# Kernel optimization log

Hardware: AMD Instinct MI355X
Metric: run time of the kernel (lower is better)

Reference implementation:

```python
import jax, jax.numpy as jnp
import numpy as np

B, N, C, H, CLS = 16, 1024, 768, 12, 1000
M = 0.5  # amax init for alpha


def setup_inputs() -> dict:
    key = jax.random.key(0)
    k = jax.random.split(key, 7)
    x = jax.random.normal(k[0], (B, N, C), jnp.float32)
    label = jax.random.randint(k[1], (B,), 0, CLS)
    # alpha is initialized to ones*m in the module; add small noise so gating is non-trivial
    alpha = jnp.ones((CLS, 3 * C), jnp.float32) * M + 0.1 * jax.random.normal(k[2], (CLS, 3 * C), jnp.float32)
    qkv_w = jax.random.normal(k[3], (3 * C, C), jnp.float32) * 0.02
    qkv_b = jax.random.normal(k[4], (3 * C,), jnp.float32) * 0.02
    proj_w = jax.random.normal(k[5], (C, C), jnp.float32) * 0.02
    proj_b = jax.random.normal(k[6], (C,), jnp.float32) * 0.02
    return {"x": x, "label": label, "alpha": alpha, "qkv_w": qkv_w,
            "qkv_b": qkv_b, "proj_w": proj_w, "proj_b": proj_b}


def reference(x, label, alpha, qkv_w, qkv_b, proj_w, proj_b):
    b, n, c = x.shape
    h = H
    hd = c // h
    scale = hd ** -0.5
    # per-sample sigmoid gate over the 3C output rows of the qkv projection
    sig = jax.nn.sigmoid(alpha[label])  # (B, 3C)
    # F.linear(x_i, W * s_i[:,None], b * s_i) == (x_i @ W.T) * s_i + b * s_i
    qkv = jnp.einsum('bnc,dc->bnd', x, qkv_w) * sig[:, None, :] + (qkv_b * sig)[:, None, :]
    qkv = qkv.reshape(b, n, 3, h, hd).transpose(2, 0, 3, 1, 4)  # (3, B, H, N, hd)
    q, k_, v = qkv[0], qkv[1], qkv[2]
    attn = jax.nn.softmax(jnp.einsum('bhqd,bhkd->bhqk', q, k_) * scale, axis=-1)
    out = jnp.einsum('bhqk,bhkd->bhqd', attn, v)          # (B, H, N, hd)
    out = out.transpose(0, 2, 1, 3).reshape(b, n, c)       # (B, N, C)
    out = out @ proj_w.T + proj_b
    return out
```

## Files before the change

kernel.cpp:

```cpp
#include <hip/hip_runtime.h>

typedef __bf16 bf16;
typedef __attribute__((ext_vector_type(8))) __bf16 bf16x8;
typedef __attribute__((ext_vector_type(4))) float floatx4;
typedef __attribute__((ext_vector_type(8))) short short8;
typedef __attribute__((ext_vector_type(4))) short short4v;
typedef unsigned short u16;

#define B_  16
#define N_  1024
#define C_  768
#define H_  12
#define HD_ 64
#define TC_ 2304
#define QSZ (B_ * H_ * N_ * HD_)

__device__ __forceinline__ u16 f2b(float f) { bf16 h = (bf16)f; return __builtin_bit_cast(u16, h); }

typedef __attribute__((address_space(1))) const unsigned int guint;
typedef __attribute__((address_space(3))) unsigned int luint;
__device__ __forceinline__ void gl16(const u16* g, u16* l) {
    __builtin_amdgcn_global_load_lds((guint*)g, (luint*)l, 16, 0, 0);
}

__global__ __launch_bounds__(256) void cvt_swz(
    const float* __restrict__ x, const float* __restrict__ qw,
    const float* __restrict__ pw, u16* __restrict__ xb,
    u16* __restrict__ qwb, u16* __restrict__ pwb)
{
    const int gid = blockIdx.x * 256 + threadIdx.x;
    const int b   = gid & 7;
    const int rb  = gid >> 3;
    const int row = rb / 12, g = rb - row * 12;
    const float* src; u16* dst; int r;
    if (row < 16384)      { src = x;  dst = xb;  r = row; }
    else if (row < 18688) { src = qw; dst = qwb; r = row - 16384; }
    else                  { src = pw; dst = pwb; r = row - 18688; }
    const float* sp = src + (size_t)r * 768 + g * 64 + b * 8;
    floatx4 a = *(const floatx4*)sp;
    floatx4 c = *(const floatx4*)(sp + 4);
    short8 v;
    v[0] = (short)f2b(a[0]); v[1] = (short)f2b(a[1]);
    v[2] = (short)f2b(a[2]); v[3] = (short)f2b(a[3]);
    v[4] = (short)f2b(c[0]); v[5] = (short)f2b(c[1]);
    v[6] = (short)f2b(c[2]); v[7] = (short)f2b(c[3]);
    *(short8*)(dst + (size_t)r * 768 + g * 64 + (b ^ (r & 7)) * 8) = v;
}

template <int MODE>
__global__ __launch_bounds__(256, 4) void gemm_bt(
    const u16* __restrict__ A, const u16* __restrict__ W,
    const float* __restrict__ bias, const float* __restrict__ alpha,
    const int* __restrict__ label, void* __restrict__ out, u16* __restrict__ vT)
{
    __shared__ __align__(16) u16 sm[16384];
    u16* sA = sm;
    u16* sB = sm + 8192;
    const int t  = threadIdx.x;
    const int w  = t >> 6, l = t & 63;
    const int lr = l & 15, lq = l >> 4;
    const int id = blockIdx.x;
    const int xcd = id & 7, j = id >> 3;
    const int m0 = (xcd * 16 + (j & 15)) << 7;
    const int n0 = (j >> 4) << 7;
    const int wm = (w >> 1) << 6, wn = (w & 1) << 6;
    const int sw = lr & 7;

    floatx4 acc[4][4];
#pragma unroll
    for (int a = 0; a < 4; a++)
#pragma unroll
        for (int b = 0; b < 4; b++) acc[a][b] = (floatx4){0.f, 0.f, 0.f, 0.f};

    const int cx8  = (t & 7) * 8;
    const int row0 = t >> 3;

    auto a_off = [&](int r, int ks) -> int {
        const int m = m0 + r;
        if (MODE == 0) return m * 768 + ks * 64 + cx8;
        return (((m >> 10) * H_ + ks) * N_ + (m & (N_ - 1))) * HD_ + cx8;
    };

    const int nk = 12;
    for (int ks = 0; ks < nk; ++ks) {
        __syncthreads();
#pragma unroll
        for (int i = 0; i < 4; i++) {
            gl16(A + a_off(row0 + 32 * i, ks), sA + i * 2048 + t * 8);
            gl16(W + (n0 + row0 + 32 * i) * 768 + ks * 64 + cx8, sB + i * 2048 + t * 8);
        }
        __syncthreads();
#pragma unroll
        for (int kc = 0; kc < 2; kc++) {
            bf16x8 af[4], bfr[4];
#pragma unroll
            for (int mt = 0; mt < 4; mt++)
                af[mt] = *(const bf16x8*)(sA + (wm + mt * 16 + lr) * 64 + 8 * ((kc * 4 + lq) ^ sw));
#pragma unroll
            for (int nt = 0; nt < 4; nt++)
                bfr[nt] = *(const bf16x8*)(sB + (wn + nt * 16 + lr) * 64 + 8 * ((kc * 4 + lq) ^ sw));
#pragma unroll
            for (int mt = 0; mt < 4; mt++)
#pragma unroll
                for (int nt = 0; nt < 4; nt++)
                    acc[mt][nt] = __builtin_amdgcn_mfma_f32_16x16x32_bf16(af[mt], bfr[nt], acc[mt][nt], 0, 0, 0);
        }
    }

    if (MODE == 0) {
        const int b   = m0 >> 10;
        const int lab = label[b];
        const int which = (n0 >= 1536) ? 2 : (n0 >= 768 ? 1 : 0);
        if (which == 2) {
#pragma unroll
            for (int nt = 0; nt < 4; nt++) {
                const int d3   = n0 + wn + nt * 16 + lr;
                const float sg = 1.f / (1.f + __expf(-alpha[lab * TC_ + d3]));
                const float bv = bias[d3];
                const int rcol = d3 - 1536;
                const int h = rcol >> 6, dd = rcol & 63;
                u16* vp = vT + (((b * H_ + h) * HD_ + dd) << 10);
#pragma unroll
                for (int mt = 0; mt < 4; mt++) {
                    const int nb = (m0 & 1023) + wm + mt * 16 + lq * 4;
                    const int sidx = (nb & ~63) + 8 * (((nb >> 3) & 7) ^ (dd & 7)) + (nb & 7);
                    short4v pk;
#pragma unroll
                    for (int i = 0; i < 4; i++) pk[i] = (short)f2b((acc[mt][nt][i] + bv) * sg);
                    *(short4v*)(vp + sidx) = pk;
                }
            }
        } else {
            float sgv[4], bvv[4];
#pragma unroll
            for (int nt = 0; nt < 4; nt++) {
                const int d3 = n0 + wn + nt * 16 + lr;
                sgv[nt] = 1.f / (1.f + __expf(-alpha[lab * TC_ + d3]));
                bvv[nt] = bias[d3];
            }
            const int hbase = (n0 - which * 768) >> 6;
            const int nb0   = m0 & 1023;
            u16* ob = (u16*)out + which * QSZ;
#pragma unroll
            for (int p = 0; p < 2; p++) {
                __syncthreads();
                if (wm == p * 64) {
#pragma unroll
                    for (int nt = 0; nt < 4; nt++) {
                        const int c = wn + nt * 16 + lr;
#pragma unroll
                        for (int mt = 0; mt < 4; mt++)
#pragma unroll
                            for (int i = 0; i < 4; i++)
                                sm[(mt * 16 + lq * 4 + i) * 132 + c] =
                                    f2b((acc[mt][nt][i] + bvv[nt]) * sgv[nt]);
                    }
                }
                __syncthreads();
#pragma unroll
                for (int hh = 0; hh < 2; hh++) {
                    u16* dsth = ob + ((((b * H_ + hbase + hh) << 10) + nb0 + p * 64) << 6);
#pragma unroll
                    for (int mi = 0; mi < 2; mi++) {
                        const int m = (t >> 3) + 32 * mi;
                        *(short8*)(dsth + m * 64 + (t & 7) * 8) =
                            *(const short8*)(sm + m * 132 + hh * 64 + 8 * ((t & 7) ^ (m & 7)));
                    }
                }
            }
        }
    } else {
        float bvv[4];
#pragma unroll
        for (int nt = 0; nt < 4; nt++) bvv[nt] = bias[n0 + wn + nt * 16 + lr];
        __syncthreads();
        float* swf = (float*)sm + w * (16 * 68);
        const int rr = l >> 2, c0 = (l & 3) * 16;
#pragma unroll
        for (int mt = 0; mt < 4; mt++) {
#pragma unroll
            for (int nt = 0; nt < 4; nt++)
#pragma unroll
                for (int i = 0; i < 4; i++)
                    swf[(lq * 4 + i) * 68 + nt * 16 + lr] = acc[mt][nt][i] + bvv[nt];
            float* drow = (float*)out + (m0 + wm + mt * 16 + rr) * 768 + n0 + wn + c0;
#pragma unroll
            for (int jj = 0; jj < 4; jj++)
                *(floatx4*)(drow + jj * 4) = *(const floatx4*)(swf + rr * 68 + c0 + jj * 4);
        }
    }
}

__global__ __launch_bounds__(256, 4) void attn_fwd(
    u16* __restrict__ qb, const u16* __restrict__ kb, const u16* __restrict__ vtb)
{
    __shared__ __align__(16) u16 sQP[64 * 64];
    __shared__ __align__(16) u16 sK[2][64 * 64];
    __shared__ __align__(16) u16 sVt[2][64 * 64];

    const int t = threadIdx.x, w = t >> 6, l = t & 63;
    const int lr = l & 15, lq = l >> 4;
    const int id = blockIdx.x;
    const int r8 = id & 7, s = id >> 3;
    const int bh = r8 * 24 + (s >> 4);
    const int q0 = (s & 15) << 6;
    const int sw = lr & 7;

    u16* qg = qb + (bh * N_ + q0) * HD_;
    gl16(qg + t * 8,        sQP + t * 8);
    gl16(qg + 2048 + t * 8, sQP + 2048 + t * 8);
    __syncthreads();
    bf16x8 qf[2];
#pragma unroll
    for (int kc = 0; kc < 2; kc++)
        qf[kc] = *(const bf16x8*)(sQP + (w * 16 + lr) * 64 + 8 * ((kc * 4 + lq) ^ sw));

    float l_run = 0.f;
    floatx4 o_acc[4];
#pragma unroll
    for (int nt = 0; nt < 4; nt++) o_acc[nt] = (floatx4){0.f, 0.f, 0.f, 0.f};

    const u16* kgb = kb + bh * (N_ * HD_);
    const u16* vgb = vtb + bh * (HD_ * N_);
    const int vrow = t >> 3, vcol = (t & 7) * 8;

    for (int kt2 = 0; kt2 < 8; ++kt2) {
        __syncthreads();
        const u16* gk = kgb + kt2 * 8192;
        gl16(gk + t * 8,        sK[0] + t * 8);
        gl16(gk + 2048 + t * 8, sK[0] + 2048 + t * 8);
        gl16(gk + 4096 + t * 8, sK[1] + t * 8);
        gl16(gk + 6144 + t * 8, sK[1] + 2048 + t * 8);
        const u16* gv = vgb + kt2 * 128;
        gl16(gv + vrow * N_ + vcol,             sVt[0] + t * 8);
        gl16(gv + (vrow + 32) * N_ + vcol,      sVt[0] + 2048 + t * 8);
        gl16(gv + vrow * N_ + 64 + vcol,        sVt[1] + t * 8);
        gl16(gv + (vrow + 32) * N_ + 64 + vcol, sVt[1] + 2048 + t * 8);
        __syncthreads();

#pragma unroll
        for (int hf = 0; hf < 2; hf++) {
            floatx4 st[4];
#pragma unroll
            for (int mt = 0; mt < 4; mt++) st[mt] = (floatx4){0.f, 0.f, 0.f, 0.f};
#pragma unroll
            for (int kc = 0; kc < 2; kc++) {
#pragma unroll
                for (int mt = 0; mt < 4; mt++) {
                    bf16x8 kf = *(const bf16x8*)(sK[hf] + (mt * 16 + lr) * 64 + 8 * ((kc * 4 + lq) ^ sw));
                    st[mt] = __builtin_amdgcn_mfma_f32_16x16x32_bf16(kf, qf[kc], st[mt], 0, 0, 0);
                }
            }
            float rs = 0.f;
            u16 pb[4][4];
#pragma unroll
            for (int mt = 0; mt < 4; mt++) {
#pragma unroll
                for (int i = 0; i < 4; i++) {
                    const float p = __expf(fmaf(st[mt][i], 0.125f, -8.0f));
                    pb[mt][i] = f2b(p);
                    rs += p;
                }
            }
            rs += __shfl_xor(rs, 16, 64);
            rs += __shfl_xor(rs, 32, 64);
            l_run += rs;
#pragma unroll
            for (int mt = 0; mt < 4; mt++) {
                short4v pk;
#pragma unroll
                for (int i = 0; i < 4; i++) pk[i] = (short)pb[mt][i];
                *(short4v*)(sQP + (w * 16 + lr) * 64 +
                            8 * ((mt * 2 + (lq >> 1)) ^ sw) + (lq & 1) * 4) = pk;
            }
#pragma unroll
            for (int kc = 0; kc < 2; kc++) {
                bf16x8 pf = *(const bf16x8*)(sQP + (w * 16 + lr) * 64 + 8 * ((kc * 4 + lq) ^ sw));
#pragma unroll
                for (int nt = 0; nt < 4; nt++) {
                    bf16x8 vf = *(const bf16x8*)(sVt[hf] + (nt * 16 + lr) * 64 + 8 * ((kc * 4 + lq) ^ sw));
                    o_acc[nt] = __builtin_amdgcn_mfma_f32_16x16x32_bf16(pf, vf, o_acc[nt], 0, 0, 0);
                }
            }
        }
    }

    const float linv = 1.f / l_run;
#pragma unroll
    for (int nt = 0; nt < 4; nt++) {
#pragma unroll
        for (int i = 0; i < 4; i++) {
            const float lv = __shfl(linv, lq * 4 + i, 64);
            const int row = w * 16 + lq * 4 + i;
            sQP[row * 64 + 8 * ((nt * 2 + (lr >> 3)) ^ (row & 7)) + (lr & 7)] = f2b(o_acc[nt][i] * lv);
        }
    }
    __syncthreads();
#pragma unroll
    for (int i2 = 0; i2 < 2; i2++) {
        const int idx = i2 * 2048 + t * 8;
        *(short8*)(qg + idx) = *(const short8*)(sQP + idx);
    }
}

extern "C" void kernel_launch(void* const* d_in, const int* in_sizes, int n_in,
                              void* d_out, int out_size, void* d_ws, size_t ws_size,
                              hipStream_t stream)
{
    const float* x      = (const float*)d_in[0];
    const int*   label  = (const int*)d_in[1];
    const float* alpha  = (const float*)d_in[2];
    const float* qkv_w  = (const float*)d_in[3];
    const float* qkv_b  = (const float*)d_in[4];
    const float* proj_w = (const float*)d_in[5];
    const float* proj_b = (const float*)d_in[6];

    u16* xb    = (u16*)d_ws;
    u16* qwb   = xb + (size_t)16384 * 768;
    u16* pwb   = qwb + (size_t)2304 * 768;
    u16* qbuf  = pwb + (size_t)768 * 768;
    u16* kbuf  = qbuf + QSZ;
    u16* vtbuf = kbuf + QSZ;

    cvt_swz<<<7296, 256, 0, stream>>>(x, qkv_w, proj_w, xb, qwb, pwb);
    gemm_bt<0><<<2304, 256, 0, stream>>>(xb, qwb, qkv_b, alpha, label, qbuf, vtbuf);
    attn_fwd<<<3072, 256, 0, stream>>>(qbuf, kbuf, vtbuf);
    gemm_bt<1><<<768, 256, 0, stream>>>(qbuf, pwb, proj_b, nullptr, nullptr, d_out, nullptr);
}
```

Before: 340.0 us.

## Double-buffer K/V tiles in attention loop with next-tile prefetch and MFMA priority

Restructures the attention main loop to process 64-key tiles. Each iteration issues async global-to-LDS loads for the next tile into the alternate buffer before computing on the current one, so load latency can overlap the QK and PV MFMAs. This replaces the old scheme of two barriers around a 128-key blocking load. It also raises wave priority around the MFMA blocks, switches the softmax exponent to exp2f with a prescaled constant, and splits the row-sum into two accumulators. The risk is that the end-of-iteration barrier still waits on the prefetch, which limits how much overlap is achieved.

```diff
diff --git a/kernel.cpp b/kernel.cpp
--- a/kernel.cpp
+++ b/kernel.cpp
@@ -206,10 +206,25 @@
     const int q0 = (s & 15) << 6;
     const int sw = lr & 7;
 
+    const u16* kgb = kb + bh * (N_ * HD_);
+    const u16* vgb = vtb + bh * (HD_ * N_);
+    const int vrow = t >> 3, vcol = (t & 7) * 8;
+
+    auto stage = [&](int kt, int bufi) {
+        const u16* gk = kgb + kt * 4096;
+        gl16(gk + t * 8,        sK[bufi] + t * 8);
+        gl16(gk + 2048 + t * 8, sK[bufi] + 2048 + t * 8);
+        const u16* gv = vgb + kt * 64;
+        gl16(gv + vrow * N_ + vcol,        sVt[bufi] + t * 8);
+        gl16(gv + (vrow + 32) * N_ + vcol, sVt[bufi] + 2048 + t * 8);
+    };
+
     u16* qg = qb + (bh * N_ + q0) * HD_;
     gl16(qg + t * 8,        sQP + t * 8);
     gl16(qg + 2048 + t * 8, sQP + 2048 + t * 8);
+    stage(0, 0);
     __syncthreads();
+
     bf16x8 qf[2];
 #pragma unroll
     for (int kc = 0; kc < 2; kc++)
@@ -220,69 +235,60 @@
 #pragma unroll
     for (int nt = 0; nt < 4; nt++) o_acc[nt] = (floatx4){0.f, 0.f, 0.f, 0.f};
 
-    const u16* kgb = kb + bh * (N_ * HD_);
-    const u16* vgb = vtb + bh * (HD_ * N_);
-    const int vrow = t >> 3, vcol = (t & 7) * 8;
-
-    for (int kt2 = 0; kt2 < 8; ++kt2) {
+#pragma unroll 2
+    for (int kt = 0; kt < 16; ++kt) {
+        const int cb = kt & 1;
+        if (kt < 15) stage(kt + 1, cb ^ 1);
+
+        floatx4 st[4];
+#pragma unroll
+        for (int mt = 0; mt < 4; mt++) st[mt] = (floatx4){0.f, 0.f, 0.f, 0.f};
+        __builtin_amdgcn_s_setprio(1);
+#pragma unroll
+        for (int kc = 0; kc < 2; kc++) {
+#pragma unroll
+            for (int mt = 0; mt < 4; mt++) {
+                bf16x8 kf = *(const bf16x8*)(sK[cb] + (mt * 16 + lr) * 64 + 8 * ((kc * 4 + lq) ^ sw));
+                st[mt] = __builtin_amdgcn_mfma_f32_16x16x32_bf16(kf, qf[kc], st[mt], 0, 0, 0);
+            }
+        }
+        __builtin_amdgcn_s_setprio(0);
+
+        float rs0 = 0.f, rs1 = 0.f;
+        u16 pb[4][4];
+#pragma unroll
+        for (int mt = 0; mt < 4; mt++) {
+#pragma unroll
+            for (int i = 0; i < 4; i++) {
+                const float p = exp2f(fmaf(st[mt][i], 0.18033688011112f, -11.54156032711171f));
+                pb[mt][i] = f2b(p);
+                if (mt & 1) rs1 += p; else rs0 += p;
+            }
+        }
+        float rs = rs0 + rs1;
+        rs += __shfl_xor(rs, 16, 64);
+        rs += __shfl_xor(rs, 32, 64);
+        l_run += rs;
+#pragma unroll
+        for (int mt = 0; mt < 4; mt++) {
+            short4v pk;
+#pragma unroll
+            for (int i = 0; i < 4; i++) pk[i] = (short)pb[mt][i];
+            *(short4v*)(sQP + (w * 16 + lr) * 64 +
+                        8 * ((mt * 2 + (lq >> 1)) ^ sw) + (lq & 1) * 4) = pk;
+        }
+        __builtin_amdgcn_s_setprio(1);
+#pragma unroll
+        for (int kc = 0; kc < 2; kc++) {
+            bf16x8 pf = *(const bf16x8*)(sQP + (w * 16 + lr) * 64 + 8 * ((kc * 4 + lq) ^ sw));
+#pragma unroll
+            for (int nt = 0; nt < 4; nt++) {
+                bf16x8 vf = *(const bf16x8*)(sVt[cb] + (nt * 16 + lr) * 64 + 8 * ((kc * 4 + lq) ^ sw));
+                o_acc[nt] = __builtin_amdgcn_mfma_f32_16x16x32_bf16(pf, vf, o_acc[nt], 0, 0, 0);
+            }
+        }
+        __builtin_amdgcn_s_setprio(0);
         __syncthreads();
-        const u16* gk = kgb + kt2 * 8192;
-        gl16(gk + t * 8,        sK[0] + t * 8);
-        gl16(gk + 2048 + t * 8, sK[0] + 2048 + t * 8);
-        gl16(gk + 4096 + t * 8, sK[1] + t * 8);
-        gl16(gk + 6144 + t * 8, sK[1] + 2048 + t * 8);
-        const u16* gv = vgb + kt2 * 128;
-        gl16(gv + vrow * N_ + vcol,             sVt[0] + t * 8);
-        gl16(gv + (vrow + 32) * N_ + vcol,      sVt[0] + 2048 + t * 8);
-        gl16(gv + vrow * N_ + 64 + vcol,        sVt[1] + t * 8);
-        gl16(gv + (vrow + 32) * N_ + 64 + vcol, sVt[1] + 2048 + t * 8);
-        __syncthreads();
-
-#pragma unroll
-        for (int hf = 0; hf < 2; hf++) {
-            floatx4 st[4];
-#pragma unroll
-            for (int mt = 0; mt < 4; mt++) st[mt] = (floatx4){0.f, 0.f, 0.f, 0.f};
-#pragma unroll
-            for (int kc = 0; kc < 2; kc++) {
-#pragma unroll
-                for (int mt = 0; mt < 4; mt++) {
-                    bf16x8 kf = *(const bf16x8*)(sK[hf] + (mt * 16 + lr) * 64 + 8 * ((kc * 4 + lq) ^ sw));
-                    st[mt] = __builtin_amdgcn_mfma_f32_16x16x32_bf16(kf, qf[kc], st[mt], 0, 0, 0);
-                }
-            }
-            float rs = 0.f;
-            u16 pb[4][4];
-#pragma unroll
-            for (int mt = 0; mt < 4; mt++) {
-#pragma unroll
-                for (int i = 0; i < 4; i++) {
-                    const float p = __expf(fmaf(st[mt][i], 0.125f, -8.0f));
-                    pb[mt][i] = f2b(p);
-                    rs += p;
-                }
-            }
-            rs += __shfl_xor(rs, 16, 64);
-            rs += __shfl_xor(rs, 32, 64);
-            l_run += rs;
-#pragma unroll
-            for (int mt = 0; mt < 4; mt++) {
-                short4v pk;
-#pragma unroll
-                for (int i = 0; i < 4; i++) pk[i] = (short)pb[mt][i];
-                *(short4v*)(sQP + (w * 16 + lr) * 64 +
-                            8 * ((mt * 2 + (lq >> 1)) ^ sw) + (lq & 1) * 4) = pk;
-            }
-#pragma unroll
-            for (int kc = 0; kc < 2; kc++) {
-                bf16x8 pf = *(const bf16x8*)(sQP + (w * 16 + lr) * 64 + 8 * ((kc * 4 + lq) ^ sw));
-#pragma unroll
-                for (int nt = 0; nt < 4; nt++) {
-                    bf16x8 vf = *(const bf16x8*)(sVt[hf] + (nt * 16 + lr) * 64 + 8 * ((kc * 4 + lq) ^ sw));
-                    o_acc[nt] = __builtin_amdgcn_mfma_f32_16x16x32_bf16(pf, vf, o_acc[nt], 0, 0, 0);
-                }
-            }
-        }
     }
 
     const float linv = 1.f / l_run;
```

Result: no change. 342.1 us (+0.6%).
